# Kernel tuning notes

Hardware: AMD Instinct MI355X
Metric: run time of the kernel (lower is better)

Reference implementation:

```python
import jax, jax.numpy as jnp
import numpy as np

V, E, C, B, T = 50257, 256, 48, 64, 1024


def setup_inputs() -> dict:
    key = jax.random.key(0)
    ks = jax.random.split(key, 8)
    x = jax.random.randint(ks[0], (B, T), 0, V)
    labels = jax.random.randint(ks[1], (B, T), 0, C)
    emb_table = jax.random.normal(ks[2], (V, E), jnp.float32) * 0.02
    fc_w = jax.random.normal(ks[3], (C, E), jnp.float32) * 0.02
    fc_b = jnp.zeros((C,), jnp.float32)
    start_trans = jax.random.normal(ks[4], (C,), jnp.float32) * 0.1
    end_trans = jax.random.normal(ks[5], (C,), jnp.float32) * 0.1
    trans = jax.random.normal(ks[6], (C, C), jnp.float32) * 0.1
    return {"x": x, "labels": labels, "emb_table": emb_table, "fc_w": fc_w,
            "fc_b": fc_b, "start_trans": start_trans, "end_trans": end_trans,
            "trans": trans}


def _crf_log_likelihood(logits, labels, start_trans, end_trans, trans):
    # logits: [B,T,C], labels: [B,T]; mask is all ones (no mask passed to torchcrf)
    # Numerator: score of the gold path.
    emit = jnp.take_along_axis(logits, labels[..., None], axis=2)[..., 0]  # [B,T]
    tr = trans[labels[:, :-1], labels[:, 1:]]                               # [B,T-1]
    numerator = (start_trans[labels[:, 0]] + emit.sum(axis=1)
                 + tr.sum(axis=1) + end_trans[labels[:, -1]])               # [B]
    # Denominator: forward algorithm (log partition) via scan over time.
    alpha0 = start_trans[None, :] + logits[:, 0]                            # [B,C]

    def step(alpha, emis_t):
        # alpha[b,i] + trans[i,j] + emis_t[b,j] -> logsumexp over i
        nxt = jax.nn.logsumexp(alpha[:, :, None] + trans[None, :, :]
                               + emis_t[:, None, :], axis=1)
        return nxt, None

    alpha, _ = jax.lax.scan(step, alpha0, jnp.swapaxes(logits[:, 1:], 0, 1))
    log_z = jax.nn.logsumexp(alpha + end_trans[None, :], axis=1)            # [B]
    return jnp.sum(numerator - log_z)  # torchcrf default reduction='sum'


def reference(x, labels, emb_table, fc_w, fc_b, start_trans, end_trans, trans):
    embed = emb_table[x]                                   # [B,T,E]
    logits = jnp.einsum('bte,ce->btc', embed, fc_w) + fc_b  # [B,T,C]
    llh = _crf_log_likelihood(logits, labels, start_trans, end_trans, trans)
    return logits, -llh
```

## Files before the change

kernel.cpp:

```cpp
#include <hip/hip_runtime.h>
#include <hip/hip_bf16.h>
#include <math.h>

#define NV 50257
#define NE 256
#define NC 48
#define NB 64
#define NT 1024
#define NCHUNK 32
#define ELD 68
#define L2E 1.44269504088896340736f
#define LN2 0.69314718055994530942f

typedef __attribute__((ext_vector_type(8)))  short bf16x8;
typedef __attribute__((ext_vector_type(16))) float f32x16;

__device__ __forceinline__ unsigned pk_bf16(float lo, float hi) {
    unsigned r;
    asm("v_cvt_pk_bf16_f32 %0, %1, %2" : "=v"(r) : "v"(lo), "v"(hi));
    return r;
}
__device__ __forceinline__ bf16x8 mk8(unsigned u0, unsigned u1, unsigned u2, unsigned u3) {
    union { unsigned u[4]; bf16x8 v; } t;
    t.u[0] = u0; t.u[1] = u1; t.u[2] = u2; t.u[3] = u3;
    return t.v;
}

__global__ __launch_bounds__(256) void logits_kernel(
    const int* __restrict__ x, const float* __restrict__ emb,
    const float* __restrict__ w, const float* __restrict__ bias,
    float* __restrict__ out, float* __restrict__ out_scalar)
{
    __shared__ __align__(16) uint4 Wf[2048];

    const int tid = threadIdx.x;
    if (blockIdx.x == 0 && tid == 0) *out_scalar = 0.f;

#pragma unroll
    for (int i = 0; i < 8; ++i) {
        const int f = i * 256 + tid;
        const int lane_ = f & 63;
        const int rt_ = (f >> 6) & 1;
        const int kf_ = f >> 7;
        const int r = (lane_ & 31) + 32 * rt_;
        const int h_ = lane_ >> 5;
        uint4 u = make_uint4(0u, 0u, 0u, 0u);
        if (r < NC) {
            const float* wr = w + r * NE + 16 * kf_ + 4 * h_;
            float4 w0 = *(const float4*)(wr);
            float4 w1 = *(const float4*)(wr + 8);
            u.x = pk_bf16(w0.x, w0.y); u.y = pk_bf16(w0.z, w0.w);
            u.z = pk_bf16(w1.x, w1.y); u.w = pk_bf16(w1.z, w1.w);
        }
        Wf[f] = u;
    }

    const int wv = tid >> 6;
    const int lane = tid & 63;
    const int l31 = lane & 31, h = lane >> 5;
    const int t = (blockIdx.x * 4 + wv) * 32 + l31;

    const float* __restrict__ erow = emb + (size_t)x[t] * NE + 4 * h;

    float4 bb[6];
#pragma unroll
    for (int g = 0; g < 4; ++g) bb[g] = *(const float4*)(bias + 8 * g + 4 * h);
#pragma unroll
    for (int g = 0; g < 2; ++g) bb[4 + g] = *(const float4*)(bias + 32 + 8 * g + 4 * h);

    __syncthreads();

    f32x16 acc0, acc1;
#pragma unroll
    for (int i = 0; i < 16; ++i) { acc0[i] = 0.f; acc1[i] = 0.f; }

    uint4 a0c = Wf[lane];
    uint4 a1c = Wf[64 + lane];
    float4 e0c = *(const float4*)(erow);
    float4 e1c = *(const float4*)(erow + 8);

#pragma unroll
    for (int kf = 0; kf < 16; ++kf) {
        uint4 a0n, a1n; float4 e0n, e1n;
        if (kf < 15) {
            a0n = Wf[(kf + 1) * 128 + lane];
            a1n = Wf[(kf + 1) * 128 + 64 + lane];
            e0n = *(const float4*)(erow + 16 * (kf + 1));
            e1n = *(const float4*)(erow + 16 * (kf + 1) + 8);
        }
        bf16x8 B = mk8(pk_bf16(e0c.x, e0c.y), pk_bf16(e0c.z, e0c.w),
                       pk_bf16(e1c.x, e1c.y), pk_bf16(e1c.z, e1c.w));
        bf16x8 A0 = mk8(a0c.x, a0c.y, a0c.z, a0c.w);
        bf16x8 A1 = mk8(a1c.x, a1c.y, a1c.z, a1c.w);
        acc0 = __builtin_amdgcn_mfma_f32_32x32x16_bf16(A0, B, acc0, 0, 0, 0);
        acc1 = __builtin_amdgcn_mfma_f32_32x32x16_bf16(A1, B, acc1, 0, 0, 0);
        if (kf < 15) { a0c = a0n; a1c = a1n; e0c = e0n; e1c = e1n; }
    }

    float* __restrict__ op = out + (size_t)t * NC;
#pragma unroll
    for (int g = 0; g < 4; ++g) {
        float4 v = make_float4(acc0[4*g+0] + bb[g].x, acc0[4*g+1] + bb[g].y,
                               acc0[4*g+2] + bb[g].z, acc0[4*g+3] + bb[g].w);
        *(float4*)(op + 8 * g + 4 * h) = v;
    }
#pragma unroll
    for (int g = 0; g < 2; ++g) {
        float4 v = make_float4(acc1[4*g+0] + bb[4+g].x, acc1[4*g+1] + bb[4+g].y,
                               acc1[4*g+2] + bb[4+g].z, acc1[4*g+3] + bb[4+g].w);
        *(float4*)(op + 32 + 8 * g + 4 * h) = v;
    }
}

__device__ __forceinline__ bf16x8 mkA(const float* __restrict__ trans, int r, int h, int kf) {
    unsigned u[4];
#pragma unroll
    for (int p = 0; p < 4; ++p) {
        const int i0 = 2 * p;
        const int k0 = 16 * kf + 4 * h + (i0 & 3) + 8 * (i0 >> 2);
        const int k1 = k0 + 1;
        float v0 = (r < NC && k0 < NC) ? exp2f(trans[k0 * NC + r] * L2E) : 0.f;
        float v1 = (r < NC && k1 < NC) ? exp2f(trans[k1 * NC + r] * L2E) : 0.f;
        u[p] = pk_bf16(v0, v1);
    }
    return mk8(u[0], u[1], u[2], u[3]);
}

__device__ __forceinline__ f32x16 mkW(const float* __restrict__ trans, int rt, int ct, int h, int l31) {
    f32x16 r;
#pragma unroll
    for (int reg = 0; reg < 16; ++reg) {
        const int rw = 32 * rt + (reg & 3) + 8 * (reg >> 2) + 4 * h;
        const int cc = 32 * ct + l31;
        r[reg] = (rw < NC && cc < NC) ? exp2f(trans[cc * NC + rw] * L2E) : 0.f;
    }
    return r;
}

__device__ __forceinline__ f32x16 mm3(bf16x8 a0, bf16x8 a1, bf16x8 a2,
                                      bf16x8 b0, bf16x8 b1, bf16x8 b2) {
    f32x16 z;
#pragma unroll
    for (int i = 0; i < 16; ++i) z[i] = 0.f;
    f32x16 d = __builtin_amdgcn_mfma_f32_32x32x16_bf16(a0, b0, z, 0, 0, 0);
    d = __builtin_amdgcn_mfma_f32_32x32x16_bf16(a1, b1, d, 0, 0, 0);
    d = __builtin_amdgcn_mfma_f32_32x32x16_bf16(a2, b2, d, 0, 0, 0);
    return d;
}

__device__ __forceinline__ void scaleRows(f32x16& A, const float* ef, int rt, int h) {
#pragma unroll
    for (int g = 0; g < 4; ++g) {
        float4 e = *(const float4*)(ef + 32 * rt + 8 * g + 4 * h);
        A[4*g+0] *= e.x; A[4*g+1] *= e.y; A[4*g+2] *= e.z; A[4*g+3] *= e.w;
    }
}

__device__ __forceinline__ void storeQ(unsigned* __restrict__ cbase, const f32x16& A,
                                       float inv, int rt, int ct, int h, int l31) {
#pragma unroll
    for (int g = 0; g < 4; ++g)
#pragma unroll
        for (int pp = 0; pp < 2; ++pp) {
            const int reg = 4 * g + 2 * pp;
            unsigned u = pk_bf16(A[reg] * inv, A[reg + 1] * inv);
            const int rw = 32 * rt + 2 * pp + 8 * g + 4 * h;
            cbase[(rw >> 1) * 64 + 32 * ct + l31] = u;
        }
}

#define MKB1(BD, S, q, eo)                                                \
  {                                                                       \
    float4 _e0 = *(const float4*)(ep + (eo));                             \
    float4 _e1 = *(const float4*)(ep + (eo) + 8);                         \
    unsigned _u0 = pk_bf16(S[(q)+0]*_e0.x, S[(q)+1]*_e0.y);               \
    unsigned _u1 = pk_bf16(S[(q)+2]*_e0.z, S[(q)+3]*_e0.w);               \
    unsigned _u2 = pk_bf16(S[(q)+4]*_e1.x, S[(q)+5]*_e1.y);               \
    unsigned _u3 = pk_bf16(S[(q)+6]*_e1.z, S[(q)+7]*_e1.w);               \
    BD = mk8(_u0, _u1, _u2, _u3);                                         \
  }

__global__ __launch_bounds__(128, 3) void scan_kernel(
    const float* __restrict__ trans, const float* __restrict__ logits,
    unsigned* __restrict__ Cpk, float* __restrict__ S2tab)
{
    const int j = blockIdx.x;
    const int b = blockIdx.y;
    const int tid = threadIdx.x;
    const int ct = tid >> 6;
    const int lane = tid & 63;
    const int h = lane >> 5, l31 = lane & 31;
    const int t0 = j * 32;
    const int cl = (j == NCHUNK - 1) ? 31 : 32;

    __shared__ __align__(16) float El[32 * ELD];
    __shared__ float mxs[2], svs[2];

    const int row = tid >> 2, cs = tid & 3;
    float s2v = 0.f;
    {
        float e[12];
        float mloc = -3.0e38f;
        if (row < cl) {
            const float* lr = logits + ((size_t)b * NT + t0 + 1 + row) * NC + cs * 12;
            float4 v0 = *(const float4*)(lr + 0);
            float4 v1 = *(const float4*)(lr + 4);
            float4 v2 = *(const float4*)(lr + 8);
            e[0]=v0.x; e[1]=v0.y; e[2]=v0.z;  e[3]=v0.w;
            e[4]=v1.x; e[5]=v1.y; e[6]=v1.z;  e[7]=v1.w;
            e[8]=v2.x; e[9]=v2.y; e[10]=v2.z; e[11]=v2.w;
#pragma unroll
            for (int q = 0; q < 12; ++q) mloc = fmaxf(mloc, e[q]);
        }
        mloc = fmaxf(mloc, __shfl_xor(mloc, 1));
        mloc = fmaxf(mloc, __shfl_xor(mloc, 2));
        const float m2 = mloc * L2E;
        float* er = El + row * ELD;
        if (row < cl) {
#pragma unroll
            for (int q = 0; q < 12; ++q) er[cs * 12 + q] = exp2f(e[q] * L2E - m2);
            if (cs == 0) s2v = m2;
        }
        if (cs == 3) {
            *(float4*)(er + 48) = make_float4(0.f, 0.f, 0.f, 0.f);
            *(float4*)(er + 52) = make_float4(0.f, 0.f, 0.f, 0.f);
            *(float4*)(er + 56) = make_float4(0.f, 0.f, 0.f, 0.f);
            *(float4*)(er + 60) = make_float4(0.f, 0.f, 0.f, 0.f);
            *(float4*)(er + 64) = make_float4(0.f, 0.f, 0.f, 0.f);
        }
    }
    __syncthreads();

    bf16x8 A00 = mkA(trans, l31,      h, 0), A01 = mkA(trans, l31,      h, 1),
           A02 = mkA(trans, l31,      h, 2);
    bf16x8 A10 = mkA(trans, l31 + 32, h, 0), A11 = mkA(trans, l31 + 32, h, 1),
           A12 = mkA(trans, l31 + 32, h, 2);

    f32x16 acc0 = mkW(trans, 0, ct, h, l31);
    f32x16 acc1 = mkW(trans, 1, ct, h, l31);

    const int nst = cl - 1;
#pragma unroll 2
    for (int s = 1; s <= nst; ++s) {
        if (s == 16) {
#pragma unroll
            for (int r = 0; r < 16; ++r) { acc0[r] *= 0x1p-88f; acc1[r] *= 0x1p-88f; }
        }
        const float* ep = El + (s - 1) * ELD;
        bf16x8 B0, B1, B2;
        MKB1(B0, acc0, 0,  0 + 4 * h);
        MKB1(B1, acc0, 8, 16 + 4 * h);
        MKB1(B2, acc1, 0, 32 + 4 * h);
        f32x16 n0 = mm3(A00, A01, A02, B0, B1, B2);
        f32x16 n1 = mm3(A10, A11, A12, B0, B1, B2);
        acc0 = n0; acc1 = n1;
    }

    const float* ef = El + nst * ELD;
    scaleRows(acc0, ef, 0, h);
    scaleRows(acc1, ef, 1, h);

    float m = acc0[0];
#pragma unroll
    for (int r = 0; r < 16; ++r) { m = fmaxf(m, acc0[r]); m = fmaxf(m, acc1[r]); }
#pragma unroll
    for (int o = 32; o; o >>= 1) m = fmaxf(m, __shfl_xor(m, o));
    float sv = s2v;
#pragma unroll
    for (int o = 32; o; o >>= 1) sv += __shfl_xor(sv, o);
    if (lane == 0) { mxs[ct] = m; svs[ct] = sv; }
    __syncthreads();
    m = fmaxf(mxs[0], mxs[1]);
    const float inv = 1.f / m;

    unsigned* cbase = Cpk + (((size_t)b * NCHUNK + j) << 11);
    storeQ(cbase, acc0, inv, 0, ct, h, l31);
    storeQ(cbase, acc1, inv, 1, ct, h, l31);

    if (tid == 0) S2tab[b * NCHUNK + j] = svs[0] + svs[1] + 88.f + log2f(m);
}

__device__ __forceinline__ void comb_load(const unsigned* __restrict__ cb, int k,
                                          uint4* __restrict__ buf) {
    const uint4* p = (const uint4*)(cb + (size_t)k * 2048);
#pragma unroll
    for (int q = 0; q < 12; ++q) buf[q] = p[q];
}

__device__ __forceinline__ void comb_step(const uint4* __restrict__ buf,
                                          float& a, unsigned sh,
                                          float* __restrict__ ash, int lane) {
    ash[lane] = a;
    __syncthreads();
    float4 av[12];
#pragma unroll
    for (int q = 0; q < 12; ++q) av[q] = *(const float4*)(ash + 4 * q);
    float a0 = 0.f, a1 = 0.f, a2 = 0.f, a3 = 0.f;
#pragma unroll
    for (int q = 0; q < 12; ++q) {
        uint4 u = buf[q];
        a0 = fmaf(__uint_as_float((u.x << sh) & 0xffff0000u), av[q].x, a0);
        a1 = fmaf(__uint_as_float((u.y << sh) & 0xffff0000u), av[q].y, a1);
        a2 = fmaf(__uint_as_float((u.z << sh) & 0xffff0000u), av[q].z, a2);
        a3 = fmaf(__uint_as_float((u.w << sh) & 0xffff0000u), av[q].w, a3);
    }
    a = (a0 + a1) + (a2 + a3);
    __syncthreads();
}

__global__ __launch_bounds__(64) void combine_kernel(
    const int* __restrict__ labels, const float* __restrict__ logits,
    const float* __restrict__ start_t, const float* __restrict__ end_t,
    const float* __restrict__ trans, const unsigned* __restrict__ Cpk,
    const float* __restrict__ S2tab, float* __restrict__ out_scalar)
{
    __shared__ __align__(16) float ash[64];
    const int b = blockIdx.x;
    const int lane = threadIdx.x;
    const int* __restrict__ lab = labels + b * NT;
    const float* __restrict__ lgp = logits + (size_t)b * NT * NC;

    float nsum = 0.f;
#pragma unroll
    for (int i = 0; i < NT / 64; ++i) {
        const int t = i * 64 + lane;
        const int l = lab[t];
        nsum += lgp[t * NC + l];
        if (t > 0) nsum += trans[lab[t - 1] * NC + l];
    }
#pragma unroll
    for (int o = 32; o; o >>= 1) nsum += __shfl_xor(nsum, o);

    float a = (lane < NC) ? exp2f((start_t[lane] + lgp[lane]) * L2E) : 0.f;
    float S2 = 0.f;
    const unsigned sh = (lane & 1) ? 0u : 16u;
    const unsigned* cb = Cpk + (((size_t)b * NCHUNK) << 11) + (lane >> 1) * 64;

    uint4 bufA[12], bufB[12];
    comb_load(cb, 0, bufA);
#pragma unroll 1
    for (int k = 0; k < NCHUNK; k += 2) {
        if (k + 1 < NCHUNK) comb_load(cb, k + 1, bufB);
        comb_step(bufA, a, sh, ash, lane);
        if (k + 2 < NCHUNK) comb_load(cb, k + 2, bufA);
        comb_step(bufB, a, sh, ash, lane);
        if ((k & 7) == 6) {
            float mm = a;
#pragma unroll
            for (int o = 32; o; o >>= 1) mm = fmaxf(mm, __shfl_xor(mm, o));
            a *= 1.f / mm;
            S2 += log2f(mm);
        }
    }

    float pe = (lane < NC) ? a * exp2f(end_t[lane] * L2E) : 0.f;
#pragma unroll
    for (int o = 32; o; o >>= 1) pe += __shfl_xor(pe, o);
    float s2k = (lane < NCHUNK) ? S2tab[b * NCHUNK + lane] : 0.f;
#pragma unroll
    for (int o = 32; o; o >>= 1) s2k += __shfl_xor(s2k, o);

    if (lane == 0) {
        const float logz = (S2 + s2k + log2f(pe)) * LN2;
        const float numer = nsum + start_t[lab[0]] + end_t[lab[NT - 1]];
        atomicAdd(out_scalar, logz - numer);
    }
}

extern "C" void kernel_launch(void* const* d_in, const int* in_sizes, int n_in,
                              void* d_out, int out_size, void* d_ws, size_t ws_size,
                              hipStream_t stream) {
    const int*   x       = (const int*)d_in[0];
    const int*   labels  = (const int*)d_in[1];
    const float* emb     = (const float*)d_in[2];
    const float* fc_w    = (const float*)d_in[3];
    const float* fc_b    = (const float*)d_in[4];
    const float* start_t = (const float*)d_in[5];
    const float* end_t   = (const float*)d_in[6];
    const float* trans   = (const float*)d_in[7];

    float* out = (float*)d_out;
    float* out_scalar = out + (size_t)NB * NT * NC;

    char* ws = (char*)d_ws;
    constexpr size_t CP_BYTES = (size_t)NB * NCHUNK * 2048 * 4;
    unsigned* Cpk   = (unsigned*)ws;
    float*    S2tab = (float*)(ws + CP_BYTES);

    logits_kernel<<<NB * NT / 128, 256, 0, stream>>>(x, emb, fc_w, fc_b, out, out_scalar);
    scan_kernel<<<dim3(NCHUNK, NB), 128, 0, stream>>>(trans, out, Cpk, S2tab);
    combine_kernel<<<NB, 64, 0, stream>>>(labels, out, start_t, end_t, trans, Cpk, S2tab, out_scalar);
}
```

Before: 72.85 us.

## Stage embedding rows through double-buffered LDS with coalesced bf16 loads

The logits kernel now loads embedding rows cooperatively: eight threads per token fetch contiguous float4 chunks, convert them to bf16 and write them into a double-buffered, padded LDS tile. MFMA operands are then read from LDS instead of each lane doing strided global float4 loads. This aims for better-coalesced gathers and overlap of the global loads with compute. The cost is two barriers per stage and extra LDS traffic and capacity, which may reduce occupancy.

```diff
diff --git a/kernel.cpp b/kernel.cpp
--- a/kernel.cpp
+++ b/kernel.cpp
@@ -32,6 +32,7 @@
     float* __restrict__ out, float* __restrict__ out_scalar)
 {
     __shared__ __align__(16) uint4 Wf[2048];
+    __shared__ __align__(16) unsigned Ebf[2][128 * 18];
 
     const int tid = threadIdx.x;
     if (blockIdx.x == 0 && tid == 0) *out_scalar = 0.f;
@@ -55,12 +56,20 @@
         Wf[f] = u;
     }
 
+    const int tloc = tid >> 3;
+    const int q    = tid & 7;
+    const float4* rp[4];
+#pragma unroll
+    for (int i = 0; i < 4; ++i) {
+        const int gt = blockIdx.x * 128 + i * 32 + tloc;
+        rp[i] = (const float4*)(emb + (size_t)x[gt] * NE) + q;
+    }
+
     const int wv = tid >> 6;
     const int lane = tid & 63;
     const int l31 = lane & 31, h = lane >> 5;
-    const int t = (blockIdx.x * 4 + wv) * 32 + l31;
-
-    const float* __restrict__ erow = emb + (size_t)x[t] * NE + 4 * h;
+    const int t = blockIdx.x * 128 + wv * 32 + l31;
+    const int t18 = (wv * 32 + l31) * 18;
 
     float4 bb[6];
 #pragma unroll
@@ -68,33 +77,46 @@
 #pragma unroll
     for (int g = 0; g < 2; ++g) bb[4 + g] = *(const float4*)(bias + 32 + 8 * g + 4 * h);
 
-    __syncthreads();
-
     f32x16 acc0, acc1;
 #pragma unroll
     for (int i = 0; i < 16; ++i) { acc0[i] = 0.f; acc1[i] = 0.f; }
 
-    uint4 a0c = Wf[lane];
-    uint4 a1c = Wf[64 + lane];
-    float4 e0c = *(const float4*)(erow);
-    float4 e1c = *(const float4*)(erow + 8);
-
-#pragma unroll
-    for (int kf = 0; kf < 16; ++kf) {
-        uint4 a0n, a1n; float4 e0n, e1n;
-        if (kf < 15) {
-            a0n = Wf[(kf + 1) * 128 + lane];
-            a1n = Wf[(kf + 1) * 128 + 64 + lane];
-            e0n = *(const float4*)(erow + 16 * (kf + 1));
-            e1n = *(const float4*)(erow + 16 * (kf + 1) + 8);
-        }
-        bf16x8 B = mk8(pk_bf16(e0c.x, e0c.y), pk_bf16(e0c.z, e0c.w),
-                       pk_bf16(e1c.x, e1c.y), pk_bf16(e1c.z, e1c.w));
-        bf16x8 A0 = mk8(a0c.x, a0c.y, a0c.z, a0c.w);
-        bf16x8 A1 = mk8(a1c.x, a1c.y, a1c.z, a1c.w);
-        acc0 = __builtin_amdgcn_mfma_f32_32x32x16_bf16(A0, B, acc0, 0, 0, 0);
-        acc1 = __builtin_amdgcn_mfma_f32_32x32x16_bf16(A1, B, acc1, 0, 0, 0);
-        if (kf < 15) { a0c = a0n; a1c = a1n; e0c = e0n; e1c = e1n; }
+    float4 st[4];
+#pragma unroll
+    for (int i = 0; i < 4; ++i) st[i] = rp[i][0];
+#pragma unroll
+    for (int i = 0; i < 4; ++i) {
+        uint2 u = make_uint2(pk_bf16(st[i].x, st[i].y), pk_bf16(st[i].z, st[i].w));
+        *(uint2*)&Ebf[0][(i * 32 + tloc) * 18 + 2 * q] = u;
+    }
+
+#pragma unroll 1
+    for (int e = 0; e < 8; ++e) {
+        __syncthreads();
+        if (e < 7) {
+#pragma unroll
+            for (int i = 0; i < 4; ++i) st[i] = rp[i][8 * (e + 1)];
+        }
+        const unsigned* eb = &Ebf[e & 1][t18];
+#pragma unroll
+        for (int kp = 0; kp < 2; ++kp) {
+            const int kf = 2 * e + kp;
+            uint2 eA = *(const uint2*)(eb + 8 * kp + 2 * h);
+            uint2 eB = *(const uint2*)(eb + 8 * kp + 2 * h + 4);
+            bf16x8 B = mk8(eA.x, eA.y, eB.x, eB.y);
+            uint4 a0 = Wf[kf * 128 + lane];
+            uint4 a1 = Wf[kf * 128 + 64 + lane];
+            acc0 = __builtin_amdgcn_mfma_f32_32x32x16_bf16(mk8(a0.x, a0.y, a0.z, a0.w), B, acc0, 0, 0, 0);
+            acc1 = __builtin_amdgcn_mfma_f32_32x32x16_bf16(mk8(a1.x, a1.y, a1.z, a1.w), B, acc1, 0, 0, 0);
+        }
+        __syncthreads();
+        if (e < 7) {
+#pragma unroll
+            for (int i = 0; i < 4; ++i) {
+                uint2 u = make_uint2(pk_bf16(st[i].x, st[i].y), pk_bf16(st[i].z, st[i].w));
+                *(uint2*)&Ebf[(e + 1) & 1][(i * 32 + tloc) * 18 + 2 * q] = u;
+            }
+        }
     }
 
     float* __restrict__ op = out + (size_t)t * NC;
@@ -210,7 +232,7 @@
             e[4]=v1.x; e[5]=v1.y; e[6]=v1.z;  e[7]=v1.w;
             e[8]=v2.x; e[9]=v2.y; e[10]=v2.z; e[11]=v2.w;
 #pragma unroll
-            for (int q = 0; q < 12; ++q) mloc = fmaxf(mloc, e[q]);
+            for (int qq = 0; qq < 12; ++qq) mloc = fmaxf(mloc, e[qq]);
         }
         mloc = fmaxf(mloc, __shfl_xor(mloc, 1));
         mloc = fmaxf(mloc, __shfl_xor(mloc, 2));
@@ -218,7 +240,7 @@
         float* er = El + row * ELD;
         if (row < cl) {
 #pragma unroll
-            for (int q = 0; q < 12; ++q) er[cs * 12 + q] = exp2f(e[q] * L2E - m2);
+            for (int qq = 0; qq < 12; ++qq) er[cs * 12 + qq] = exp2f(e[qq] * L2E - m2);
             if (cs == 0) s2v = m2;
         }
         if (cs == 3) {
```

New measurement: 72.12 us. No clear change (-1.0%).

## Fuse embedding-projection GEMM into chunked CRF scan kernel, precompute weight fragments

Applied to the files above, without the earlier changes.

The logits GEMM moves into the scan kernel. Each block computes the logits for its own 32-step chunk in registers, writes them out, and builds the exponentiated emission tile straight from the MFMA accumulators instead of reading logits back from global memory. Both waves compute the GEMM: the second wave computes the previous chunk's tokens and writes overlapping rows. A tiny prep kernel converts the FC weights to bf16 fragments once, and the gold-path emission sum is produced per chunk so the combine kernel no longer gathers from logits. This saves a logits round trip and a launch, but adds redundant GEMM work and duplicate stores, and gives the scan kernel more register pressure.

```diff
diff --git a/kernel.cpp b/kernel.cpp
--- a/kernel.cpp
+++ b/kernel.cpp
@@ -26,16 +26,12 @@
     return t.v;
 }
 
-__global__ __launch_bounds__(256) void logits_kernel(
-    const int* __restrict__ x, const float* __restrict__ emb,
-    const float* __restrict__ w, const float* __restrict__ bias,
-    float* __restrict__ out, float* __restrict__ out_scalar)
+__global__ __launch_bounds__(256) void prep_kernel(
+    const float* __restrict__ w, uint4* __restrict__ Wfrag,
+    float* __restrict__ out_scalar)
 {
-    __shared__ __align__(16) uint4 Wf[2048];
-
     const int tid = threadIdx.x;
-    if (blockIdx.x == 0 && tid == 0) *out_scalar = 0.f;
-
+    if (tid == 0) *out_scalar = 0.f;
 #pragma unroll
     for (int i = 0; i < 8; ++i) {
         const int f = i * 256 + tid;
@@ -52,63 +48,7 @@
             u.x = pk_bf16(w0.x, w0.y); u.y = pk_bf16(w0.z, w0.w);
             u.z = pk_bf16(w1.x, w1.y); u.w = pk_bf16(w1.z, w1.w);
         }
-        Wf[f] = u;
-    }
-
-    const int wv = tid >> 6;
-    const int lane = tid & 63;
-    const int l31 = lane & 31, h = lane >> 5;
-    const int t = (blockIdx.x * 4 + wv) * 32 + l31;
-
-    const float* __restrict__ erow = emb + (size_t)x[t] * NE + 4 * h;
-
-    float4 bb[6];
-#pragma unroll
-    for (int g = 0; g < 4; ++g) bb[g] = *(const float4*)(bias + 8 * g + 4 * h);
-#pragma unroll
-    for (int g = 0; g < 2; ++g) bb[4 + g] = *(const float4*)(bias + 32 + 8 * g + 4 * h);
-
-    __syncthreads();
-
-    f32x16 acc0, acc1;
-#pragma unroll
-    for (int i = 0; i < 16; ++i) { acc0[i] = 0.f; acc1[i] = 0.f; }
-
-    uint4 a0c = Wf[lane];
-    uint4 a1c = Wf[64 + lane];
-    float4 e0c = *(const float4*)(erow);
-    float4 e1c = *(const float4*)(erow + 8);
-
-#pragma unroll
-    for (int kf = 0; kf < 16; ++kf) {
-        uint4 a0n, a1n; float4 e0n, e1n;
-        if (kf < 15) {
-            a0n = Wf[(kf + 1) * 128 + lane];
-            a1n = Wf[(kf + 1) * 128 + 64 + lane];
-            e0n = *(const float4*)(erow + 16 * (kf + 1));
-            e1n = *(const float4*)(erow + 16 * (kf + 1) + 8);
-        }
-        bf16x8 B = mk8(pk_bf16(e0c.x, e0c.y), pk_bf16(e0c.z, e0c.w),
-                       pk_bf16(e1c.x, e1c.y), pk_bf16(e1c.z, e1c.w));
-        bf16x8 A0 = mk8(a0c.x, a0c.y, a0c.z, a0c.w);
-        bf16x8 A1 = mk8(a1c.x, a1c.y, a1c.z, a1c.w);
-        acc0 = __builtin_amdgcn_mfma_f32_32x32x16_bf16(A0, B, acc0, 0, 0, 0);
-        acc1 = __builtin_amdgcn_mfma_f32_32x32x16_bf16(A1, B, acc1, 0, 0, 0);
-        if (kf < 15) { a0c = a0n; a1c = a1n; e0c = e0n; e1c = e1n; }
-    }
-
-    float* __restrict__ op = out + (size_t)t * NC;
-#pragma unroll
-    for (int g = 0; g < 4; ++g) {
-        float4 v = make_float4(acc0[4*g+0] + bb[g].x, acc0[4*g+1] + bb[g].y,
-                               acc0[4*g+2] + bb[g].z, acc0[4*g+3] + bb[g].w);
-        *(float4*)(op + 8 * g + 4 * h) = v;
-    }
-#pragma unroll
-    for (int g = 0; g < 2; ++g) {
-        float4 v = make_float4(acc1[4*g+0] + bb[4+g].x, acc1[4*g+1] + bb[4+g].y,
-                               acc1[4*g+2] + bb[4+g].z, acc1[4*g+3] + bb[4+g].w);
-        *(float4*)(op + 32 + 8 * g + 4 * h) = v;
+        Wfrag[f] = u;
     }
 }
 
@@ -181,7 +121,10 @@
   }
 
 __global__ __launch_bounds__(128, 3) void scan_kernel(
-    const float* __restrict__ trans, const float* __restrict__ logits,
+    const float* __restrict__ trans, const int* __restrict__ x,
+    const int* __restrict__ labels, const float* __restrict__ emb,
+    const float* __restrict__ bias, const uint4* __restrict__ Wfrag,
+    float* __restrict__ out, float* __restrict__ nsum_part,
     unsigned* __restrict__ Cpk, float* __restrict__ S2tab)
 {
     const int j = blockIdx.x;
@@ -194,40 +137,117 @@
     const int cl = (j == NCHUNK - 1) ? 31 : 32;
 
     __shared__ __align__(16) float El[32 * ELD];
-    __shared__ float mxs[2], svs[2];
-
-    const int row = tid >> 2, cs = tid & 3;
-    float s2v = 0.f;
+    __shared__ float mxs[2], svs_sh;
+
+    const int tok_raw = (ct == 0) ? (t0 + 1 + l31) : (t0 - 31 + l31);
+    const int tokc = min(max(tok_raw, 0), NT - 1);
+    const float* __restrict__ erow = emb + (size_t)x[b * NT + tokc] * NE + 4 * h;
+
+    float4 bb[6];
+#pragma unroll
+    for (int g = 0; g < 4; ++g) bb[g] = *(const float4*)(bias + 8 * g + 4 * h);
+#pragma unroll
+    for (int g = 0; g < 2; ++g) bb[4 + g] = *(const float4*)(bias + 32 + 8 * g + 4 * h);
+
+    f32x16 acc0, acc1;
+#pragma unroll
+    for (int i = 0; i < 16; ++i) { acc0[i] = 0.f; acc1[i] = 0.f; }
+
+    uint4 a0c = Wfrag[lane], a1c = Wfrag[64 + lane];
+    float4 e0c = *(const float4*)(erow);
+    float4 e1c = *(const float4*)(erow + 8);
+#pragma unroll
+    for (int kf = 0; kf < 16; ++kf) {
+        uint4 a0n, a1n; float4 e0n, e1n;
+        if (kf < 15) {
+            a0n = Wfrag[(kf + 1) * 128 + lane];
+            a1n = Wfrag[(kf + 1) * 128 + 64 + lane];
+            e0n = *(const float4*)(erow + 16 * (kf + 1));
+            e1n = *(const float4*)(erow + 16 * (kf + 1) + 8);
+        }
+        bf16x8 B = mk8(pk_bf16(e0c.x, e0c.y), pk_bf16(e0c.z, e0c.w),
+                       pk_bf16(e1c.x, e1c.y), pk_bf16(e1c.z, e1c.w));
+        acc0 = __builtin_amdgcn_mfma_f32_32x32x16_bf16(mk8(a0c.x, a0c.y, a0c.z, a0c.w), B, acc0, 0, 0, 0);
+        acc1 = __builtin_amdgcn_mfma_f32_32x32x16_bf16(mk8(a1c.x, a1c.y, a1c.z, a1c.w), B, acc1, 0, 0, 0);
+        if (kf < 15) { a0c = a0n; a1c = a1n; e0c = e0n; e1c = e1n; }
+    }
+
+#pragma unroll
+    for (int g = 0; g < 4; ++g) {
+        acc0[4*g+0] += bb[g].x; acc0[4*g+1] += bb[g].y;
+        acc0[4*g+2] += bb[g].z; acc0[4*g+3] += bb[g].w;
+    }
+#pragma unroll
+    for (int g = 0; g < 2; ++g) {
+        acc1[4*g+0] += bb[4+g].x; acc1[4*g+1] += bb[4+g].y;
+        acc1[4*g+2] += bb[4+g].z; acc1[4*g+3] += bb[4+g].w;
+    }
+
     {
-        float e[12];
-        float mloc = -3.0e38f;
-        if (row < cl) {
-            const float* lr = logits + ((size_t)b * NT + t0 + 1 + row) * NC + cs * 12;
-            float4 v0 = *(const float4*)(lr + 0);
-            float4 v1 = *(const float4*)(lr + 4);
-            float4 v2 = *(const float4*)(lr + 8);
-            e[0]=v0.x; e[1]=v0.y; e[2]=v0.z;  e[3]=v0.w;
-            e[4]=v1.x; e[5]=v1.y; e[6]=v1.z;  e[7]=v1.w;
-            e[8]=v2.x; e[9]=v2.y; e[10]=v2.z; e[11]=v2.w;
-#pragma unroll
-            for (int q = 0; q < 12; ++q) mloc = fmaxf(mloc, e[q]);
-        }
-        mloc = fmaxf(mloc, __shfl_xor(mloc, 1));
-        mloc = fmaxf(mloc, __shfl_xor(mloc, 2));
+        float* __restrict__ op = out + ((size_t)b * NT + tokc) * NC;
+#pragma unroll
+        for (int g = 0; g < 4; ++g)
+            *(float4*)(op + 8 * g + 4 * h) =
+                make_float4(acc0[4*g+0], acc0[4*g+1], acc0[4*g+2], acc0[4*g+3]);
+#pragma unroll
+        for (int g = 0; g < 2; ++g)
+            *(float4*)(op + 32 + 8 * g + 4 * h) =
+                make_float4(acc1[4*g+0], acc1[4*g+1], acc1[4*g+2], acc1[4*g+3]);
+    }
+
+    float sv = 0.f;
+    if (ct == 0) {
+        float mloc = acc0[0];
+#pragma unroll
+        for (int r = 1; r < 16; ++r) mloc = fmaxf(mloc, acc0[r]);
+#pragma unroll
+        for (int r = 0; r < 8; ++r) mloc = fmaxf(mloc, acc1[r]);
+        mloc = fmaxf(mloc, __shfl_xor(mloc, 32));
         const float m2 = mloc * L2E;
-        float* er = El + row * ELD;
-        if (row < cl) {
-#pragma unroll
-            for (int q = 0; q < 12; ++q) er[cs * 12 + q] = exp2f(e[q] * L2E - m2);
-            if (cs == 0) s2v = m2;
-        }
-        if (cs == 3) {
-            *(float4*)(er + 48) = make_float4(0.f, 0.f, 0.f, 0.f);
-            *(float4*)(er + 52) = make_float4(0.f, 0.f, 0.f, 0.f);
-            *(float4*)(er + 56) = make_float4(0.f, 0.f, 0.f, 0.f);
-            *(float4*)(er + 60) = make_float4(0.f, 0.f, 0.f, 0.f);
-            *(float4*)(er + 64) = make_float4(0.f, 0.f, 0.f, 0.f);
-        }
+
+        float* er = El + l31 * ELD;
+#pragma unroll
+        for (int reg = 0; reg < 16; ++reg) {
+            const int cls = (reg & 3) + 8 * (reg >> 2) + 4 * h;
+            er[cls] = exp2f(acc0[reg] * L2E - m2);
+        }
+#pragma unroll
+        for (int reg = 0; reg < 8; ++reg) {
+            const int cls = 32 + (reg & 3) + 8 * (reg >> 2) + 4 * h;
+            er[cls] = exp2f(acc1[reg] * L2E - m2);
+        }
+#pragma unroll
+        for (int reg = 8; reg < 16; ++reg) {
+            const int cls = 32 + (reg & 3) + 8 * (reg >> 2) + 4 * h;
+            er[cls] = 0.f;
+        }
+        if (ELD > 64 && h == 0) {
+            er[64] = 0.f; er[65] = 0.f; er[66] = 0.f; er[67] = 0.f;
+        }
+        if (h == 0 && l31 < cl) sv = m2;
+
+        {
+            const int lt = labels[b * NT + tokc];
+            float ev = 0.f;
+            if (l31 < cl && (((lt >> 2) & 1) == h)) {
+                const int rt_sel = lt >> 5;
+                const int rr = (lt & 31) - 4 * h;
+                const int regidx = (rr & 3) + 4 * (rr >> 3);
+                float av = 0.f;
+#pragma unroll
+                for (int reg = 0; reg < 16; ++reg) {
+                    av = (rt_sel == 0 && reg == regidx) ? acc0[reg] : av;
+                    av = (rt_sel == 1 && reg == regidx) ? acc1[reg] : av;
+                }
+                ev = av;
+            }
+#pragma unroll
+            for (int o = 32; o; o >>= 1) ev += __shfl_xor(ev, o);
+            if (lane == 0) nsum_part[b * NCHUNK + j] = ev;
+        }
+#pragma unroll
+        for (int o = 32; o; o >>= 1) sv += __shfl_xor(sv, o);
+        if (lane == 0) svs_sh = sv;
     }
     __syncthreads();
 
@@ -236,48 +256,45 @@
     bf16x8 A10 = mkA(trans, l31 + 32, h, 0), A11 = mkA(trans, l31 + 32, h, 1),
            A12 = mkA(trans, l31 + 32, h, 2);
 
-    f32x16 acc0 = mkW(trans, 0, ct, h, l31);
-    f32x16 acc1 = mkW(trans, 1, ct, h, l31);
+    f32x16 s_acc0 = mkW(trans, 0, ct, h, l31);
+    f32x16 s_acc1 = mkW(trans, 1, ct, h, l31);
 
     const int nst = cl - 1;
 #pragma unroll 2
     for (int s = 1; s <= nst; ++s) {
         if (s == 16) {
 #pragma unroll
-            for (int r = 0; r < 16; ++r) { acc0[r] *= 0x1p-88f; acc1[r] *= 0x1p-88f; }
+            for (int r = 0; r < 16; ++r) { s_acc0[r] *= 0x1p-88f; s_acc1[r] *= 0x1p-88f; }
         }
         const float* ep = El + (s - 1) * ELD;
         bf16x8 B0, B1, B2;
-        MKB1(B0, acc0, 0,  0 + 4 * h);
-        MKB1(B1, acc0, 8, 16 + 4 * h);
-        MKB1(B2, acc1, 0, 32 + 4 * h);
+        MKB1(B0, s_acc0, 0,  0 + 4 * h);
+        MKB1(B1, s_acc0, 8, 16 + 4 * h);
+        MKB1(B2, s_acc1, 0, 32 + 4 * h);
         f32x16 n0 = mm3(A00, A01, A02, B0, B1, B2);
         f32x16 n1 = mm3(A10, A11, A12, B0, B1, B2);
-        acc0 = n0; acc1 = n1;
+        s_acc0 = n0; s_acc1 = n1;
     }
 
     const float* ef = El + nst * ELD;
-    scaleRows(acc0, ef, 0, h);
-    scaleRows(acc1, ef, 1, h);
-
-    float m = acc0[0];
-#pragma unroll
-    for (int r = 0; r < 16; ++r) { m = fmaxf(m, acc0[r]); m = fmaxf(m, acc1[r]); }
+    scaleRows(s_acc0, ef, 0, h);
+    scaleRows(s_acc1, ef, 1, h);
+
+    float m = s_acc0[0];
+#pragma unroll
+    for (int r = 0; r < 16; ++r) { m = fmaxf(m, s_acc0[r]); m = fmaxf(m, s_acc1[r]); }
 #pragma unroll
     for (int o = 32; o; o >>= 1) m = fmaxf(m, __shfl_xor(m, o));
-    float sv = s2v;
-#pragma unroll
-    for (int o = 32; o; o >>= 1) sv += __shfl_xor(sv, o);
-    if (lane == 0) { mxs[ct] = m; svs[ct] = sv; }
+    if (lane == 0) mxs[ct] = m;
     __syncthreads();
     m = fmaxf(mxs[0], mxs[1]);
     const float inv = 1.f / m;
 
     unsigned* cbase = Cpk + (((size_t)b * NCHUNK + j) << 11);
-    storeQ(cbase, acc0, inv, 0, ct, h, l31);
-    storeQ(cbase, acc1, inv, 1, ct, h, l31);
-
-    if (tid == 0) S2tab[b * NCHUNK + j] = svs[0] + svs[1] + 88.f + log2f(m);
+    storeQ(cbase, s_acc0, inv, 0, ct, h, l31);
+    storeQ(cbase, s_acc1, inv, 1, ct, h, l31);
+
+    if (tid == 0) S2tab[b * NCHUNK + j] = svs_sh + 88.f + log2f(m);
 }
 
 __device__ __forceinline__ void comb_load(const unsigned* __restrict__ cb, int k,
@@ -312,7 +329,8 @@
     const int* __restrict__ labels, const float* __restrict__ logits,
     const float* __restrict__ start_t, const float* __restrict__ end_t,
     const float* __restrict__ trans, const unsigned* __restrict__ Cpk,
-    const float* __restrict__ S2tab, float* __restrict__ out_scalar)
+    const float* __restrict__ S2tab, const float* __restrict__ nsum_part,
+    float* __restrict__ out_scalar)
 {
     __shared__ __align__(16) float ash[64];
     const int b = blockIdx.x;
@@ -324,10 +342,9 @@
 #pragma unroll
     for (int i = 0; i < NT / 64; ++i) {
         const int t = i * 64 + lane;
-        const int l = lab[t];
-        nsum += lgp[t * NC + l];
-        if (t > 0) nsum += trans[lab[t - 1] * NC + l];
-    }
+        if (t > 0) nsum += trans[lab[t - 1] * NC + lab[t]];
+    }
+    if (lane < NCHUNK) nsum += nsum_part[b * NCHUNK + lane];
 #pragma unroll
     for (int o = 32; o; o >>= 1) nsum += __shfl_xor(nsum, o);
 
@@ -362,7 +379,7 @@
 
     if (lane == 0) {
         const float logz = (S2 + s2k + log2f(pe)) * LN2;
-        const float numer = nsum + start_t[lab[0]] + end_t[lab[NT - 1]];
+        const float numer = nsum + lgp[lab[0]] + start_t[lab[0]] + end_t[lab[NT - 1]];
         atomicAdd(out_scalar, logz - numer);
     }
 }
@@ -384,10 +401,16 @@
 
     char* ws = (char*)d_ws;
     constexpr size_t CP_BYTES = (size_t)NB * NCHUNK * 2048 * 4;
-    unsigned* Cpk   = (unsigned*)ws;
-    float*    S2tab = (float*)(ws + CP_BYTES);
-
-    logits_kernel<<<NB * NT / 128, 256, 0, stream>>>(x, emb, fc_w, fc_b, out, out_scalar);
-    scan_kernel<<<dim3(NCHUNK, NB), 128, 0, stream>>>(trans, out, Cpk, S2tab);
-    combine_kernel<<<NB, 64, 0, stream>>>(labels, out, start_t, end_t, trans, Cpk, S2tab, out_scalar);
-}
+    constexpr size_t S2_BYTES = (size_t)NB * NCHUNK * 4;
+    constexpr size_t NP_BYTES = (size_t)NB * NCHUNK * 4;
+    unsigned* Cpk       = (unsigned*)ws;
+    float*    S2tab     = (float*)(ws + CP_BYTES);
+    float*    nsum_part = (float*)(ws + CP_BYTES + S2_BYTES);
+    uint4*    Wfrag     = (uint4*)(ws + CP_BYTES + S2_BYTES + NP_BYTES);
+
+    prep_kernel<<<1, 256, 0, stream>>>(fc_w, Wfrag, out_scalar);
+    scan_kernel<<<dim3(NCHUNK, NB), 128, 0, stream>>>(trans, x, labels, emb, fc_b,
+                                                      Wfrag, out, nsum_part, Cpk, S2tab);
+    combine_kernel<<<NB, 64, 0, stream>>>(labels, out, start_t, end_t, trans,
+                                          Cpk, S2tab, nsum_part, out_scalar);
+}
```

After: 83.31 us. 1.14x slower.
